# Kernel tuning notes

Measured on AMD Instinct MI355X. Metric: run time of the kernel, lower is better.

Reference implementation:

```python
import jax, jax.numpy as jnp
import numpy as np

ALPHA = 0.2  # leaky_relu negative slope
NEG_INF = -1e9


def setup_inputs() -> dict:
    key = jax.random.key(0)
    ks = jax.random.split(key, 8)
    B, U, N, Din, H, HD = 8, 1024, 2048, 128, 4, 32
    return {
        "user_features": jax.random.normal(ks[0], (B, U, Din), jnp.float32),
        "news_features": jax.random.normal(ks[1], (B, N, Din), jnp.float32),
        "adjacency": jax.random.randint(ks[2], (B, U + N, U + N), 0, 2, jnp.int32),
        "W_user": jax.random.normal(ks[3], (H, Din, HD), jnp.float32) * 0.1,
        "W_news": jax.random.normal(ks[4], (H, Din, HD), jnp.float32) * 0.1,
        "a_user_news": jax.random.normal(ks[5], (H, 2 * HD, 1), jnp.float32) * 0.1,
        "a_news_user": jax.random.normal(ks[6], (H, 2 * HD, 1), jnp.float32) * 0.1,
        "b_user": jnp.zeros((H * HD,), jnp.float32),
        "b_news": jnp.zeros((H * HD,), jnp.float32),
    }


def _attention(q, k, a, mask):
    # q: (B,H,Q,hd), k: (B,H,K,hd), a: (H,2*hd,1), mask: (B,Q,K)
    # Additive score decomposed: [q;k] @ a == q@a_q + k@a_k (same math,
    # avoids materializing the (B,H,Q,K,2hd) concat tensor).
    hd = q.shape[-1]
    a_q = a[:, :hd, 0]  # (H,hd)
    a_k = a[:, hd:, 0]  # (H,hd)
    e_q = jnp.einsum("bhqd,hd->bhq", q, a_q)
    e_k = jnp.einsum("bhkd,hd->bhk", k, a_k)
    scores = e_q[..., :, None] + e_k[..., None, :]  # (B,H,Q,K)
    scores = jnp.where(scores > 0, scores, ALPHA * scores)  # leaky_relu
    scores = jnp.where(mask[:, None, :, :] > 0, scores, NEG_INF)
    return jax.nn.softmax(scores, axis=-1)


def reference(user_features, news_features, adjacency, W_user, W_news,
              a_user_news, a_news_user, b_user, b_news):
    B, U, _ = user_features.shape
    N = news_features.shape[1]
    units = b_user.shape[0]
    user_to_news = adjacency[:, :U, U:]   # (B,U,N)
    news_to_user = adjacency[:, U:, :U]   # (B,N,U)

    q_user = jnp.einsum("bud,hdk->bhuk", user_features, W_user)  # (B,H,U,hd)
    k_news = jnp.einsum("bnd,hdk->bhnk", news_features, W_news)  # (B,H,N,hd)

    attn_un = _attention(q_user, k_news, a_user_news, user_to_news)  # (B,H,U,N)
    user_updates = jnp.einsum("bhun,bhnk->bhuk", attn_un, k_news)

    attn_nu = _attention(k_news, q_user, a_news_user, news_to_user)  # (B,H,N,U)
    news_updates = jnp.einsum("bhnu,bhuk->bhnk", attn_nu, q_user)

    # concat_heads=True: original does a raw reshape of (B,H,*,hd) -> (B,*,units)
    updated_users = jnp.reshape(user_updates, (B, U, units)) + b_user
    updated_news = jnp.reshape(news_updates, (B, N, units)) + b_news
    updated_users = jax.nn.relu(updated_users)
    updated_news = jax.nn.relu(updated_news)
    return updated_users, updated_news
```

## Files before the change

kernel.cpp:

```cpp
#include <hip/hip_runtime.h>
#include <hip/hip_bf16.h>

typedef _Float16 half8 __attribute__((ext_vector_type(8)));
typedef __fp16 fp16x2 __attribute__((ext_vector_type(2)));
typedef float f32x4 __attribute__((ext_vector_type(4)));

#define B_ 8
#define U_ 1024
#define N_ 2048
#define DIN 128
#define H_ 4
#define HD 32
#define S_ 3072
#define LOG2E 1.44269504f

__global__ __launch_bounds__(256) void p1_kernel(
    const float* __restrict__ uf, const float* __restrict__ nf,
    const float* __restrict__ Wu, const float* __restrict__ Wn,
    const float* __restrict__ a_un, const float* __restrict__ a_nu,
    _Float16* __restrict__ vtA, _Float16* __restrict__ vtB,
    float* __restrict__ eRowA, float2* __restrict__ eColA2,
    float* __restrict__ eRowB, float2* __restrict__ eColB2)
{
  __shared__ float fs[64][132];
  __shared__ float WsT[32][132];
  __shared__ float qt[32][65];
  __shared__ float aAs[32], aBs[32];

  const int bid = blockIdx.x;
  const int tid = threadIdx.x;

  int b, rt, R, h;
  const float *feat, *W;
  _Float16* vt;
  float* eRaw;
  float2* ePair;
  bool part0raw;
  int aAoff, aBoff;
  const float *avA, *avB;
  if (bid < 512) {
    h = bid & 3; int t2 = bid >> 2; b = t2 >> 4; rt = t2 & 15; R = U_;
    feat = uf; W = Wu; vt = vtB;
    eRaw = eRowA; ePair = eColB2; part0raw = true;
    avA = a_un; aAoff = 0;  avB = a_nu; aBoff = HD;
  } else {
    int t3 = bid - 512;
    h = t3 & 3; int t2 = t3 >> 2; b = t2 >> 5; rt = t2 & 31; R = N_;
    feat = nf; W = Wn; vt = vtA;
    eRaw = eRowB; ePair = eColA2; part0raw = false;
    avA = a_un; aAoff = HD; avB = a_nu; aBoff = 0;
  }
  const int r0 = rt * 64;

  const float4* feat4 = (const float4*)(feat + ((size_t)b * R + r0) * DIN);
  #pragma unroll
  for (int i = 0; i < 8; ++i) {
    int f4 = tid + 256 * i;
    int row = f4 >> 5, c4 = f4 & 31;
    *(float4*)&fs[row][c4 * 4] = feat4[row * 32 + c4];
  }
  {
    const float4* W4 = (const float4*)(W + (size_t)h * DIN * HD);
    #pragma unroll
    for (int i = 0; i < 4; ++i) {
      int f4 = tid + 256 * i;
      int d = f4 >> 3, kc = f4 & 7;
      float4 v = W4[f4];
      WsT[kc * 4 + 0][d] = v.x;
      WsT[kc * 4 + 1][d] = v.y;
      WsT[kc * 4 + 2][d] = v.z;
      WsT[kc * 4 + 3][d] = v.w;
    }
    if (tid < 32) {
      aAs[tid] = avA[h * 64 + aAoff + tid];
      aBs[tid] = avB[h * 64 + aBoff + tid];
    }
  }
  __syncthreads();

  const int kk = tid & 15, uu = tid >> 4;
  {
    float acc0[4] = {0.f, 0.f, 0.f, 0.f}, acc1[4] = {0.f, 0.f, 0.f, 0.f};
    #pragma unroll 8
    for (int d = 0; d < DIN; d += 4) {
      float4 w0 = *(const float4*)&WsT[kk][d];
      float4 w1 = *(const float4*)&WsT[kk + 16][d];
      #pragma unroll
      for (int i = 0; i < 4; ++i) {
        float4 fv = *(const float4*)&fs[uu + 16 * i][d];
        acc0[i] = fmaf(fv.x, w0.x, acc0[i]); acc0[i] = fmaf(fv.y, w0.y, acc0[i]);
        acc0[i] = fmaf(fv.z, w0.z, acc0[i]); acc0[i] = fmaf(fv.w, w0.w, acc0[i]);
        acc1[i] = fmaf(fv.x, w1.x, acc1[i]); acc1[i] = fmaf(fv.y, w1.y, acc1[i]);
        acc1[i] = fmaf(fv.z, w1.z, acc1[i]); acc1[i] = fmaf(fv.w, w1.w, acc1[i]);
      }
    }
    #pragma unroll
    for (int i = 0; i < 4; ++i) {
      qt[kk][uu + 16 * i] = acc0[i];
      qt[kk + 16][uu + 16 * i] = acc1[i];
    }
  }
  __syncthreads();

  const int u2 = tid & 63, part = tid >> 6;
  {
    size_t vtbase = (size_t)(b * H_ + h) * (R * HD)
                  + (size_t)((r0 >> 5) + (u2 >> 5)) * (HD * 32) + (u2 & 31);
    #pragma unroll
    for (int jj = 0; jj < 8; ++jj) {
      int krow = part * 8 + jj;
      vt[vtbase + krow * 32] = (_Float16)qt[krow][u2];
    }
  }
  if (part < 2) {
    float a_ = 0.f;
    const float* av = (part == 0) ? aAs : aBs;
    #pragma unroll
    for (int k2 = 0; k2 < HD; ++k2)
      a_ = fmaf(qt[k2][u2], av[k2], a_);
    float e = a_ * LOG2E;
    size_t idx = (size_t)(b * H_ + h) * R + r0 + u2;
    bool raw = (part == 0) ? part0raw : !part0raw;
    if (raw) eRaw[idx] = e;
    else     ePair[idx] = make_float2(exp2f(e), exp2f(0.2f * e));
  }
}

struct Tile { float4 e0, e1, e2, e3; half8 v0, v1; unsigned int mb; };

__device__ __forceinline__ Tile load_tile(
    int t, int cg, int row16,
    const float2* __restrict__ ecol2, const _Float16* __restrict__ vtb,
    const unsigned int* maskW, int mrow)
{
  Tile ti;
  const int cb = t * 32 + cg;
  const float4* ep = (const float4*)(ecol2 + cb);
  ti.e0 = ep[0]; ti.e1 = ep[1]; ti.e2 = ep[2]; ti.e3 = ep[3];
  ti.v0 = *(const half8*)(vtb + t * (HD * 32) + row16 * 32 + cg);
  ti.v1 = *(const half8*)(vtb + t * (HD * 32) + (row16 + 16) * 32 + cg);
  ti.mb = maskW[mrow + t] >> cg;
  return ti;
}

__device__ __forceinline__ void compute_tile(
    const Tile& ti, float F1, float F2, float G, half8 ones,
    f32x4& acc0, f32x4& acc1, f32x4& accd)
{
  float wv[8];
  wv[0] = (ti.mb & 1u)   ? (ti.e0.x > G ? ti.e0.x * F1 : ti.e0.y * F2) : 0.f;
  wv[1] = (ti.mb & 2u)   ? (ti.e0.z > G ? ti.e0.z * F1 : ti.e0.w * F2) : 0.f;
  wv[2] = (ti.mb & 4u)   ? (ti.e1.x > G ? ti.e1.x * F1 : ti.e1.y * F2) : 0.f;
  wv[3] = (ti.mb & 8u)   ? (ti.e1.z > G ? ti.e1.z * F1 : ti.e1.w * F2) : 0.f;
  wv[4] = (ti.mb & 16u)  ? (ti.e2.x > G ? ti.e2.x * F1 : ti.e2.y * F2) : 0.f;
  wv[5] = (ti.mb & 32u)  ? (ti.e2.z > G ? ti.e2.z * F1 : ti.e2.w * F2) : 0.f;
  wv[6] = (ti.mb & 64u)  ? (ti.e3.x > G ? ti.e3.x * F1 : ti.e3.y * F2) : 0.f;
  wv[7] = (ti.mb & 128u) ? (ti.e3.z > G ? ti.e3.z * F1 : ti.e3.w * F2) : 0.f;
  union { fp16x2 h2[4]; half8 h8; } uw;
  uw.h2[0] = __builtin_amdgcn_cvt_pkrtz(wv[0], wv[1]);
  uw.h2[1] = __builtin_amdgcn_cvt_pkrtz(wv[2], wv[3]);
  uw.h2[2] = __builtin_amdgcn_cvt_pkrtz(wv[4], wv[5]);
  uw.h2[3] = __builtin_amdgcn_cvt_pkrtz(wv[6], wv[7]);
  half8 w = uw.h8;
  acc0 = __builtin_amdgcn_mfma_f32_16x16x32_f16(w, ti.v0, acc0, 0, 0, 0);
  acc1 = __builtin_amdgcn_mfma_f32_16x16x32_f16(w, ti.v1, acc1, 0, 0, 0);
  accd = __builtin_amdgcn_mfma_f32_16x16x32_f16(w, ones, accd, 0, 0, 0);
}

template<int RR, int CC, int ROFF, int COFF, int PAD64>
__device__ __forceinline__ void p2_core(
    int b, int rt, int wave, int l,
    const int* __restrict__ adj, const _Float16* __restrict__ vt,
    const float* __restrict__ eRow, const float2* __restrict__ eCol2,
    const float* __restrict__ bias, float* __restrict__ out,
    unsigned long long* maskU)
{
  constexpr int CW64 = CC / 64;

  const int* adjBase = adj + (size_t)b * S_ * S_ + (size_t)(ROFF + rt * 16) * S_ + COFF;
  #pragma unroll 4
  for (int i = 0; i < (16 * CW64) / 4; ++i) {
    int f = i * 4 + wave;
    int row = f / CW64, chunk = f % CW64;
    int av = adjBase[(size_t)row * S_ + chunk * 64 + l];
    unsigned long long m = __ballot(av != 0);
    if (l == 0) maskU[row * PAD64 + chunk] = m;
  }
  __syncthreads();

  const int h = wave;
  const int row16 = l & 15;
  const int cg = (l >> 4) << 3;
  const int r = rt * 16 + row16;
  const float eq = eRow[(size_t)(b * H_ + h) * RR + r];
  const float F1 = exp2f(eq), F2 = exp2f(0.2f * eq), G = exp2f(-eq);
  const float2* ecol2 = eCol2 + (size_t)(b * H_ + h) * CC;
  const _Float16* vtb = vt + (size_t)(b * H_ + h) * (CC * HD);
  const unsigned int* maskW = (const unsigned int*)maskU;
  const int mrow = row16 * (PAD64 * 2);

  f32x4 acc0 = {0.f,0.f,0.f,0.f}, acc1 = {0.f,0.f,0.f,0.f}, accd = {0.f,0.f,0.f,0.f};
  half8 ones = {(_Float16)1.f, (_Float16)1.f, (_Float16)1.f, (_Float16)1.f,
                (_Float16)1.f, (_Float16)1.f, (_Float16)1.f, (_Float16)1.f};

  constexpr int T = CC / 32;
  Tile cur = load_tile(0, cg, row16, ecol2, vtb, maskW, mrow);
  #pragma unroll 2
  for (int t = 0; t < T - 1; ++t) {
    Tile nxt = load_tile(t + 1, cg, row16, ecol2, vtb, maskW, mrow);
    compute_tile(cur, F1, F2, G, ones, acc0, acc1, accd);
    cur = nxt;
  }
  compute_tile(cur, F1, F2, G, ones, acc0, acc1, accd);

  const int colk = row16;
  const int rowbase = rt * 16 + ((l >> 4) << 2);
  #pragma unroll
  for (int q = 0; q < 4; ++q) {
    int orow = rowbase + q;
    size_t o = ((size_t)(b * H_ + h) * RR + orow) * 32 + colk;
    float den = accd[q];
    float v0 = acc0[q] / den + bias[q * 32 + colk];
    float v1 = acc1[q] / den + bias[q * 32 + colk + 16];
    out[o]      = v0 > 0.f ? v0 : 0.f;
    out[o + 16] = v1 > 0.f ? v1 : 0.f;
  }
}

__global__ __launch_bounds__(256, 4) void p2_kernel(
    const int* __restrict__ adj,
    const _Float16* __restrict__ vtA, const _Float16* __restrict__ vtB,
    const float* __restrict__ eRowA, const float2* __restrict__ eColA2,
    const float* __restrict__ eRowB, const float2* __restrict__ eColB2,
    const float* __restrict__ bu, const float* __restrict__ bn,
    float* __restrict__ out)
{
  __shared__ unsigned long long maskU[16 * 33];
  const int tid = threadIdx.x;
  const int wave = tid >> 6, l = tid & 63;
  const int bid = blockIdx.x;
  if (bid < B_ * (U_ / 16)) {
    const int b = bid & 7, rt = bid >> 3;
    p2_core<U_, N_, 0, U_, 33>(b, rt, wave, l, adj, vtA, eRowA, eColA2, bu,
                               out, maskU);
  } else {
    const int t2 = bid - B_ * (U_ / 16);
    const int b = t2 & 7, rt = t2 >> 3;
    p2_core<N_, U_, U_, 0, 17>(b, rt, wave, l, adj, vtB, eRowB, eColB2, bn,
                               out + (size_t)B_ * U_ * 128, maskU);
  }
}

extern "C" void kernel_launch(void* const* d_in, const int* in_sizes, int n_in,
                              void* d_out, int out_size, void* d_ws, size_t ws_size,
                              hipStream_t stream) {
  const float* uf  = (const float*)d_in[0];
  const float* nf  = (const float*)d_in[1];
  const int*   adj = (const int*)d_in[2];
  const float* Wu  = (const float*)d_in[3];
  const float* Wn  = (const float*)d_in[4];
  const float* aun = (const float*)d_in[5];
  const float* anu = (const float*)d_in[6];
  const float* bu  = (const float*)d_in[7];
  const float* bn  = (const float*)d_in[8];

  char* ws = (char*)d_ws;
  size_t off = 0;
  _Float16* vtA = (_Float16*)(ws + off); off += (size_t)B_ * H_ * HD * N_ * 2;
  _Float16* vtB = (_Float16*)(ws + off); off += (size_t)B_ * H_ * HD * U_ * 2;
  float*  eRowA  = (float*)(ws + off);  off += (size_t)B_ * H_ * U_ * 4;
  float2* eColA2 = (float2*)(ws + off); off += (size_t)B_ * H_ * N_ * 8;
  float*  eRowB  = (float*)(ws + off);  off += (size_t)B_ * H_ * N_ * 4;
  float2* eColB2 = (float2*)(ws + off); off += (size_t)B_ * H_ * U_ * 8;
  (void)off; (void)ws_size; (void)in_sizes; (void)n_in; (void)out_size;

  p1_kernel<<<512 + 1024, 256, 0, stream>>>(uf, nf, Wu, Wn, aun, anu,
                                            vtA, vtB, eRowA, eColA2, eRowB, eColB2);
  p2_kernel<<<B_ * (U_ / 16) + B_ * (N_ / 16), 256, 0, stream>>>(
      adj, vtA, vtB, eRowA, eColA2, eRowB, eColB2, bu, bn, (float*)d_out);
}
```

Measured before the change: 136.1 us.

## Precompute adjacency bitmasks in a separate pass before attention kernel

```diff
diff --git a/kernel.cpp b/kernel.cpp
--- a/kernel.cpp
+++ b/kernel.cpp
@@ -13,6 +13,38 @@
 #define HD 32
 #define S_ 3072
 #define LOG2E 1.44269504f
+
+__global__ __launch_bounds__(256) void p0_kernel(
+    const int* __restrict__ adj,
+    unsigned int* __restrict__ mA, unsigned int* __restrict__ mB)
+{
+  const int task = blockIdx.x * 4 + (threadIdx.x >> 6);
+  const int l = threadIdx.x & 63;
+  const int* rowp;
+  unsigned int* mOut;
+  int iters;
+  if (task < 8192) {
+    int b = task >> 10, r = task & 1023;
+    rowp = adj + ((size_t)b * S_ + r) * S_ + U_;
+    iters = 32;
+    mOut = mA + ((size_t)(b * 64 + (r >> 4)) * 64) * 16 + (r & 15);
+  } else {
+    int t2 = task - 8192;
+    int b = t2 >> 11, r = t2 & 2047;
+    rowp = adj + ((size_t)b * S_ + U_ + r) * S_;
+    iters = 16;
+    mOut = mB + ((size_t)(b * 128 + (r >> 4)) * 32) * 16 + (r & 15);
+  }
+  #pragma unroll 4
+  for (int it = 0; it < iters; ++it) {
+    int av = rowp[it * 64 + l];
+    unsigned long long m = __ballot(av != 0);
+    if (l == 0) {
+      mOut[(2 * it) * 16]     = (unsigned int)m;
+      mOut[(2 * it + 1) * 16] = (unsigned int)(m >> 32);
+    }
+  }
+}
 
 __global__ __launch_bounds__(256) void p1_kernel(
     const float* __restrict__ uf, const float* __restrict__ nf,
@@ -126,12 +158,12 @@
   }
 }
 
-struct Tile { float4 e0, e1, e2, e3; half8 v0, v1; unsigned int mb; };
+struct Tile { float4 e0, e1, e2, e3; half8 v0, v1; unsigned int m32; };
 
 __device__ __forceinline__ Tile load_tile(
     int t, int cg, int row16,
     const float2* __restrict__ ecol2, const _Float16* __restrict__ vtb,
-    const unsigned int* maskW, int mrow)
+    const unsigned int* __restrict__ mT)
 {
   Tile ti;
   const int cb = t * 32 + cg;
@@ -139,23 +171,24 @@
   ti.e0 = ep[0]; ti.e1 = ep[1]; ti.e2 = ep[2]; ti.e3 = ep[3];
   ti.v0 = *(const half8*)(vtb + t * (HD * 32) + row16 * 32 + cg);
   ti.v1 = *(const half8*)(vtb + t * (HD * 32) + (row16 + 16) * 32 + cg);
-  ti.mb = maskW[mrow + t] >> cg;
+  ti.m32 = mT[t * 16 + row16];
   return ti;
 }
 
 __device__ __forceinline__ void compute_tile(
-    const Tile& ti, float F1, float F2, float G, half8 ones,
+    const Tile& ti, int cg, float F1, float F2, float G, half8 ones,
     f32x4& acc0, f32x4& acc1, f32x4& accd)
 {
+  const unsigned int mb = ti.m32 >> cg;
   float wv[8];
-  wv[0] = (ti.mb & 1u)   ? (ti.e0.x > G ? ti.e0.x * F1 : ti.e0.y * F2) : 0.f;
-  wv[1] = (ti.mb & 2u)   ? (ti.e0.z > G ? ti.e0.z * F1 : ti.e0.w * F2) : 0.f;
-  wv[2] = (ti.mb & 4u)   ? (ti.e1.x > G ? ti.e1.x * F1 : ti.e1.y * F2) : 0.f;
-  wv[3] = (ti.mb & 8u)   ? (ti.e1.z > G ? ti.e1.z * F1 : ti.e1.w * F2) : 0.f;
-  wv[4] = (ti.mb & 16u)  ? (ti.e2.x > G ? ti.e2.x * F1 : ti.e2.y * F2) : 0.f;
-  wv[5] = (ti.mb & 32u)  ? (ti.e2.z > G ? ti.e2.z * F1 : ti.e2.w * F2) : 0.f;
-  wv[6] = (ti.mb & 64u)  ? (ti.e3.x > G ? ti.e3.x * F1 : ti.e3.y * F2) : 0.f;
-  wv[7] = (ti.mb & 128u) ? (ti.e3.z > G ? ti.e3.z * F1 : ti.e3.w * F2) : 0.f;
+  wv[0] = (mb & 1u)   ? (ti.e0.x > G ? ti.e0.x * F1 : ti.e0.y * F2) : 0.f;
+  wv[1] = (mb & 2u)   ? (ti.e0.z > G ? ti.e0.z * F1 : ti.e0.w * F2) : 0.f;
+  wv[2] = (mb & 4u)   ? (ti.e1.x > G ? ti.e1.x * F1 : ti.e1.y * F2) : 0.f;
+  wv[3] = (mb & 8u)   ? (ti.e1.z > G ? ti.e1.z * F1 : ti.e1.w * F2) : 0.f;
+  wv[4] = (mb & 16u)  ? (ti.e2.x > G ? ti.e2.x * F1 : ti.e2.y * F2) : 0.f;
+  wv[5] = (mb & 32u)  ? (ti.e2.z > G ? ti.e2.z * F1 : ti.e2.w * F2) : 0.f;
+  wv[6] = (mb & 64u)  ? (ti.e3.x > G ? ti.e3.x * F1 : ti.e3.y * F2) : 0.f;
+  wv[7] = (mb & 128u) ? (ti.e3.z > G ? ti.e3.z * F1 : ti.e3.w * F2) : 0.f;
   union { fp16x2 h2[4]; half8 h8; } uw;
   uw.h2[0] = __builtin_amdgcn_cvt_pkrtz(wv[0], wv[1]);
   uw.h2[1] = __builtin_amdgcn_cvt_pkrtz(wv[2], wv[3]);
@@ -167,27 +200,13 @@
   accd = __builtin_amdgcn_mfma_f32_16x16x32_f16(w, ones, accd, 0, 0, 0);
 }
 
-template<int RR, int CC, int ROFF, int COFF, int PAD64>
+template<int RR, int CC>
 __device__ __forceinline__ void p2_core(
     int b, int rt, int wave, int l,
-    const int* __restrict__ adj, const _Float16* __restrict__ vt,
+    const unsigned int* __restrict__ mT, const _Float16* __restrict__ vt,
     const float* __restrict__ eRow, const float2* __restrict__ eCol2,
-    const float* __restrict__ bias, float* __restrict__ out,
-    unsigned long long* maskU)
-{
-  constexpr int CW64 = CC / 64;
-
-  const int* adjBase = adj + (size_t)b * S_ * S_ + (size_t)(ROFF + rt * 16) * S_ + COFF;
-  #pragma unroll 4
-  for (int i = 0; i < (16 * CW64) / 4; ++i) {
-    int f = i * 4 + wave;
-    int row = f / CW64, chunk = f % CW64;
-    int av = adjBase[(size_t)row * S_ + chunk * 64 + l];
-    unsigned long long m = __ballot(av != 0);
-    if (l == 0) maskU[row * PAD64 + chunk] = m;
-  }
-  __syncthreads();
-
+    const float* __restrict__ bias, float* __restrict__ out)
+{
   const int h = wave;
   const int row16 = l & 15;
   const int cg = (l >> 4) << 3;
@@ -196,22 +215,20 @@
   const float F1 = exp2f(eq), F2 = exp2f(0.2f * eq), G = exp2f(-eq);
   const float2* ecol2 = eCol2 + (size_t)(b * H_ + h) * CC;
   const _Float16* vtb = vt + (size_t)(b * H_ + h) * (CC * HD);
-  const unsigned int* maskW = (const unsigned int*)maskU;
-  const int mrow = row16 * (PAD64 * 2);
 
   f32x4 acc0 = {0.f,0.f,0.f,0.f}, acc1 = {0.f,0.f,0.f,0.f}, accd = {0.f,0.f,0.f,0.f};
   half8 ones = {(_Float16)1.f, (_Float16)1.f, (_Float16)1.f, (_Float16)1.f,
                 (_Float16)1.f, (_Float16)1.f, (_Float16)1.f, (_Float16)1.f};
 
   constexpr int T = CC / 32;
-  Tile cur = load_tile(0, cg, row16, ecol2, vtb, maskW, mrow);
+  Tile cur = load_tile(0, cg, row16, ecol2, vtb, mT);
   #pragma unroll 2
   for (int t = 0; t < T - 1; ++t) {
-    Tile nxt = load_tile(t + 1, cg, row16, ecol2, vtb, maskW, mrow);
-    compute_tile(cur, F1, F2, G, ones, acc0, acc1, accd);
+    Tile nxt = load_tile(t + 1, cg, row16, ecol2, vtb, mT);
+    compute_tile(cur, cg, F1, F2, G, ones, acc0, acc1, accd);
     cur = nxt;
   }
-  compute_tile(cur, F1, F2, G, ones, acc0, acc1, accd);
+  compute_tile(cur, cg, F1, F2, G, ones, acc0, acc1, accd);
 
   const int colk = row16;
   const int rowbase = rt * 16 + ((l >> 4) << 2);
@@ -228,26 +245,26 @@
 }
 
 __global__ __launch_bounds__(256, 4) void p2_kernel(
-    const int* __restrict__ adj,
+    const unsigned int* __restrict__ mA, const unsigned int* __restrict__ mB,
     const _Float16* __restrict__ vtA, const _Float16* __restrict__ vtB,
     const float* __restrict__ eRowA, const float2* __restrict__ eColA2,
     const float* __restrict__ eRowB, const float2* __restrict__ eColB2,
     const float* __restrict__ bu, const float* __restrict__ bn,
     float* __restrict__ out)
 {
-  __shared__ unsigned long long maskU[16 * 33];
   const int tid = threadIdx.x;
   const int wave = tid >> 6, l = tid & 63;
   const int bid = blockIdx.x;
   if (bid < B_ * (U_ / 16)) {
     const int b = bid & 7, rt = bid >> 3;
-    p2_core<U_, N_, 0, U_, 33>(b, rt, wave, l, adj, vtA, eRowA, eColA2, bu,
-                               out, maskU);
+    const unsigned int* mT = mA + ((size_t)(b * 64 + rt) * 64) * 16;
+    p2_core<U_, N_>(b, rt, wave, l, mT, vtA, eRowA, eColA2, bu, out);
   } else {
     const int t2 = bid - B_ * (U_ / 16);
     const int b = t2 & 7, rt = t2 >> 3;
-    p2_core<N_, U_, U_, 0, 17>(b, rt, wave, l, adj, vtB, eRowB, eColB2, bn,
-                               out + (size_t)B_ * U_ * 128, maskU);
+    const unsigned int* mT = mB + ((size_t)(b * 128 + rt) * 32) * 16;
+    p2_core<N_, U_>(b, rt, wave, l, mT, vtB, eRowB, eColB2, bn,
+                    out + (size_t)B_ * U_ * 128);
   }
 }
 
@@ -272,10 +289,13 @@
   float2* eColA2 = (float2*)(ws + off); off += (size_t)B_ * H_ * N_ * 8;
   float*  eRowB  = (float*)(ws + off);  off += (size_t)B_ * H_ * N_ * 4;
   float2* eColB2 = (float2*)(ws + off); off += (size_t)B_ * H_ * U_ * 8;
+  unsigned int* mA = (unsigned int*)(ws + off); off += (size_t)B_ * 64 * 64 * 16 * 4;
+  unsigned int* mB = (unsigned int*)(ws + off); off += (size_t)B_ * 128 * 32 * 16 * 4;
   (void)off; (void)ws_size; (void)in_sizes; (void)n_in; (void)out_size;
 
+  p0_kernel<<<6144, 256, 0, stream>>>(adj, mA, mB);
   p1_kernel<<<512 + 1024, 256, 0, stream>>>(uf, nf, Wu, Wn, aun, anu,
                                             vtA, vtB, eRowA, eColA2, eRowB, eColB2);
   p2_kernel<<<B_ * (U_ / 16) + B_ * (N_ / 16), 256, 0, stream>>>(
-      adj, vtA, vtB, eRowA, eColA2, eRowB, eColB2, bu, bn, (float*)d_out);
-}
+      mA, mB, vtA, vtB, eRowA, eColA2, eRowB, eColB2, bu, bn, (float*)d_out);
+}
```

Result: no change. 136.1 us (+0.0%).
